# Kernel optimization log

Hardware: AMD Instinct MI355X
Metric: run time of the kernel (lower is better)

Reference implementation:

```python
import jax, jax.numpy as jnp
import numpy as np

NUM_GRAPHS = 64
NODE_SZ = 200
FEAT = 200
HID = 256          # hidden_size; each signed branch outputs HID//2
HALF = HID // 2
N_NODES = NUM_GRAPHS * NODE_SZ
N_EDGES = 409600
NUM_LAYERS = 3


def _lin_init(key, out_f, in_f):
    kw, kb = jax.random.split(key)
    s = 1.0 / np.sqrt(in_f)
    W = jax.random.uniform(kw, (out_f, in_f), minval=-s, maxval=s, dtype=jnp.float32)
    b = jax.random.uniform(kb, (out_f,), minval=-s, maxval=s, dtype=jnp.float32)
    return W, b


def setup_inputs() -> dict:
    key = jax.random.key(0)
    ks = jax.random.split(key, 16)
    x = jax.random.normal(ks[0], (N_NODES, FEAT), dtype=jnp.float32)
    edge_index = jax.random.randint(ks[1], (2, N_EDGES), 0, N_NODES, dtype=jnp.int64)
    edge_weight = jax.random.normal(ks[2], (N_EDGES,), dtype=jnp.float32)
    batch = jnp.repeat(jnp.arange(NUM_GRAPHS, dtype=jnp.int64), NODE_SZ)

    # signed conv layer params: layer0 in=FEAT, layers 1..: in=HID; each lin maps 2*in -> HALF
    Wp0, bp0 = _lin_init(ks[3], HALF, 2 * FEAT)
    Wn0, bn0 = _lin_init(ks[4], HALF, 2 * FEAT)
    Wp1, bp1 = _lin_init(ks[5], HALF, 2 * HID)
    Wn1, bn1 = _lin_init(ks[6], HALF, 2 * HID)
    Wp2, bp2 = _lin_init(ks[7], HALF, 2 * HID)
    Wn2, bn2 = _lin_init(ks[8], HALF, 2 * HID)
    Wr, br = _lin_init(ks[9], HID, NODE_SZ * HID)   # readout_lin
    Wl, bl = _lin_init(ks[10], 1, HID)              # final lin
    return dict(x=x, edge_index=edge_index, edge_weight=edge_weight, batch=batch,
                Wp0=Wp0, bp0=bp0, Wn0=Wn0, bn0=bn0,
                Wp1=Wp1, bp1=bp1, Wn1=Wn1, bn1=bn1,
                Wp2=Wp2, bp2=bp2, Wn2=Wn2, bn2=bn2,
                Wr=Wr, br=br, Wl=Wl, bl=bl)


def _signed_conv(x, src, dst, w, Wp, bp, Wn, bn):
    # edge-weighted signed mean aggregation, split by weight sign
    xs = x[src]                                   # [E, D] gather
    pw = jnp.where(w > 0, w, 0.0)
    nw = jnp.where(w < 0, -w, 0.0)
    agg_p = jax.ops.segment_sum(pw[:, None] * xs, dst, num_segments=N_NODES)
    agg_n = jax.ops.segment_sum(nw[:, None] * xs, dst, num_segments=N_NODES)
    deg_p = jax.ops.segment_sum((w > 0).astype(x.dtype), dst, num_segments=N_NODES)
    deg_n = jax.ops.segment_sum((w < 0).astype(x.dtype), dst, num_segments=N_NODES)
    agg_p = agg_p / jnp.maximum(deg_p, 1.0)[:, None]
    agg_n = agg_n / jnp.maximum(deg_n, 1.0)[:, None]
    hp = jnp.concatenate([agg_p, x], -1) @ Wp.T + bp
    hn = jnp.concatenate([agg_n, x], -1) @ Wn.T + bn
    return jnp.concatenate([hp, hn], -1)          # [N, HID]


def reference(x, edge_index, edge_weight, batch,
              Wp0, bp0, Wn0, bn0, Wp1, bp1, Wn1, bn1, Wp2, bp2, Wn2, bn2,
              Wr, br, Wl, bl):
    src, dst = edge_index[0], edge_index[1]
    convs = [(Wp0, bp0, Wn0, bn0), (Wp1, bp1, Wn1, bn1), (Wp2, bp2, Wn2, bn2)]
    h = x
    for i, (Wp, bp, Wn, bn) in enumerate(convs):
        h = _signed_conv(h, src, dst, edge_weight, Wp, bp, Wn, bn)
        if i < NUM_LAYERS - 1:
            h = jax.nn.leaky_relu(h, negative_slope=0.01)
    # per-graph readout: batch is contiguous with NODE_SZ nodes per graph,
    # so the boolean-mask+view loop is exactly a reshape.
    g = h.reshape(NUM_GRAPHS, NODE_SZ * HID)
    g = g @ Wr.T + br                             # [G, HID]
    # dropout(p=0.5) is identity in eval mode
    return g @ Wl.T + bl                          # [G, 1]
```

## Files before the change

### kernel.cpp

```cpp
#include <hip/hip_runtime.h>

#define NUM_GRAPHS 64
#define NODE_SZ    200
#define FEAT       200
#define HID        256
#define HALF       128
#define N_NODES    (NUM_GRAPHS * NODE_SZ)
#define KREAD      (NODE_SZ * HID)

typedef unsigned short ushort_t;
typedef unsigned int uint_t;
typedef __attribute__((ext_vector_type(8))) short bf16x8;
typedef __attribute__((ext_vector_type(4))) float f32x4;

#define GAS(p) ((const __attribute__((address_space(1))) void*)(p))
#define LAS(p) ((__attribute__((address_space(3))) void*)(p))

__device__ __forceinline__ float bf2f(ushort_t u) {
    union { unsigned int i; float f; } v; v.i = ((unsigned int)u) << 16; return v.f;
}
__device__ __forceinline__ ushort_t f2bf(float f) {
    union { float f; unsigned int i; } v; v.f = f;
    unsigned int x = v.i;
    unsigned int r = (x + 0x7fffu + ((x >> 16) & 1u)) >> 16;
    return (ushort_t)r;
}

#define OFF_CNT    0
#define OFF_WEFF   51264
#define OFF_ES     256064
#define OFF_YALL   13363264
#define OFF_HA     26470464
#define OFF_HB     33024064
#define OFF_WALL   39577664
#define OFF_XB     40364096

__global__ __launch_bounds__(256) void prep_kernel(
        const float* __restrict__ Wp0, const float* __restrict__ Wn0,
        const float* __restrict__ Wp1, const float* __restrict__ Wn1,
        const float* __restrict__ Wp2, const float* __restrict__ Wn2,
        const float* __restrict__ x, const float* __restrict__ Wr,
        const float* __restrict__ Wl, const float* __restrict__ br,
        const float* __restrict__ bl,
        ushort_t* __restrict__ wall, ushort_t* __restrict__ xb,
        float* __restrict__ weff, float* __restrict__ outg) {
    int bx = blockIdx.x, tid = threadIdx.x;
    if (bx < 200) {
        int k = bx * 256 + tid;
        float s[16];
#pragma unroll
        for (int j = 0; j < 16; ++j) s[j] = 0.f;
#pragma unroll 1
        for (int c = 0; c < 256; c += 16) {
#pragma unroll
            for (int j = 0; j < 16; ++j)
                s[j] = fmaf(Wl[c + j], Wr[(size_t)(c + j) * KREAD + k], s[j]);
        }
        float t0 = ((s[0] + s[1]) + (s[2] + s[3])) + ((s[4] + s[5]) + (s[6] + s[7]));
        float t1 = ((s[8] + s[9]) + (s[10] + s[11])) + ((s[12] + s[13]) + (s[14] + s[15]));
        weff[k] = t0 + t1;
    } else if (bx < 300) {
        for (int idx = (bx - 200) * 256 + tid; idx < N_NODES * 64; idx += 25600) {
            int n = idx >> 6, c0 = (idx & 63) * 4;
            ushort4 o = {0, 0, 0, 0};
            if (c0 < 200) {
                float4 v = *(const float4*)&x[(size_t)n * 200 + c0];
                o.x = f2bf(v.x); o.y = f2bf(v.y); o.z = f2bf(v.z); o.w = f2bf(v.w);
            }
            *(ushort4*)&xb[(size_t)n * 256 + c0] = o;
        }
    } else if (bx < 364) {
        for (int idx = (bx - 300) * 256 + tid; idx < 3 * 131072; idx += 16384) {
            int layer = idx >> 17, within = idx & 131071;
            int rr = within >> 8, col = within & 255;
            const float* Wp = (layer == 0) ? Wp0 : (layer == 1) ? Wp1 : Wp2;
            const float* Wn = (layer == 0) ? Wn0 : (layer == 1) ? Wn1 : Wn2;
            int Ks = (layer == 0) ? 200 : 256;
            int q = rr >> 7;
            const float* Wsrc = (q & 1) ? Wn : Wp;
            int row = rr & 127;
            int scol = col + ((q >> 1) ? Ks : 0);
            float v = (col < Ks) ? Wsrc[(size_t)row * (2 * Ks) + scol] : 0.0f;
            wall[idx] = f2bf(v);
        }
    } else {
        if (tid < 64) {
            float p = br[tid] * Wl[tid] + br[tid + 64] * Wl[tid + 64]
                    + br[tid + 128] * Wl[tid + 128] + br[tid + 192] * Wl[tid + 192];
#pragma unroll
            for (int d = 32; d > 0; d >>= 1) p += __shfl_xor(p, d);
            outg[tid] = p + bl[0];
        }
    }
}

__device__ __forceinline__ void gemm_body(int t, const ushort_t* __restrict__ A,
                                          const ushort_t* __restrict__ Bw,
                                          ushort_t* __restrict__ Y,
                                          ushort_t* smem) {
    int mBase = (t >> 1) * 128;
    int nBase = (t & 1) * 256;
    int tid  = threadIdx.x;
    int lane = tid & 63;
    int wv   = tid >> 6;
    int r    = lane & 15;
    int quad = lane >> 4;
    int wm   = wv >> 1;
    int wn   = wv & 1;

    int rowA = tid >> 2, colc = (tid & 3) * 8;
    const ushort_t* gA  = A  + (size_t)(mBase + rowA) * 256 + colc;
    const ushort_t* gB0 = Bw + (size_t)(nBase + rowA) * 256 + colc;
    const ushort_t* gB1 = Bw + (size_t)(nBase + 128 + rowA) * 256 + colc;

    f32x4 acc[2][8];
#pragma unroll
    for (int i = 0; i < 2; ++i)
#pragma unroll
        for (int j = 0; j < 8; ++j) acc[i][j] = (f32x4){0.f, 0.f, 0.f, 0.f};

    auto STAGE = [&](int buf, int kb) {
        ushort_t* Ad = smem + (buf << 12) + tid * 8;
        ushort_t* Bd = smem + 8192 + (buf << 13) + tid * 8;
        __builtin_amdgcn_global_load_lds(GAS(gA + kb), LAS(Ad), 16, 0, 0);
        __builtin_amdgcn_global_load_lds(GAS(gB0 + kb), LAS(Bd), 16, 0, 0);
        __builtin_amdgcn_global_load_lds(GAS(gB1 + kb), LAS(Bd + 4096), 16, 0, 0);
    };

    STAGE(0, 0);
    for (int kt = 0; kt < 8; ++kt) {
        int cb = kt & 1;
        __syncthreads();
        if (kt < 7) STAGE(cb ^ 1, (kt + 1) * 32);
        const ushort_t* Ac = smem + (cb << 12);
        const ushort_t* Bc = smem + 8192 + (cb << 13);
        bf16x8 af[2];
#pragma unroll
        for (int i = 0; i < 2; ++i)
            af[i] = *(const bf16x8*)&Ac[(wm * 32 + i * 16 + r) * 32 + quad * 8];
#pragma unroll
        for (int j = 0; j < 8; ++j) {
            bf16x8 bfr = *(const bf16x8*)&Bc[(wn * 128 + j * 16 + r) * 32 + quad * 8];
            acc[0][j] = __builtin_amdgcn_mfma_f32_16x16x32_bf16(af[0], bfr, acc[0][j], 0, 0, 0);
            acc[1][j] = __builtin_amdgcn_mfma_f32_16x16x32_bf16(af[1], bfr, acc[1][j], 0, 0, 0);
        }
    }
#pragma unroll
    for (int i = 0; i < 2; ++i)
#pragma unroll
        for (int j = 0; j < 8; ++j) {
            int c = nBase + wn * 128 + j * 16 + r;
#pragma unroll
            for (int reg = 0; reg < 4; ++reg) {
                int m = mBase + wm * 32 + i * 16 + quad * 4 + reg;
                Y[(size_t)m * 512 + c] = f2bf(acc[i][j][reg]);
            }
        }
}

__global__ __launch_bounds__(512) void scatgemm_kernel(
        const int* __restrict__ ei, const float* __restrict__ ew,
        uint_t* __restrict__ cnt, uint2* __restrict__ es, int E,
        const ushort_t* __restrict__ xb, const ushort_t* __restrict__ wall,
        ushort_t* __restrict__ Yall) {
    __shared__ __align__(16) ushort_t smem[24576];
    int bx = blockIdx.x;
    if (bx < 200) {
        gemm_body(bx, xb, wall, Yall, smem);
        return;
    }
    int e = (bx - 200) * 512 + threadIdx.x;
    if (e < E) {
        int src = ei[e];
        int dst = ei[E + e];
        float w = ew[e];
        if (w > 0.0f) {
            uint_t old = atomicAdd(&cnt[dst], 1u);
            uint_t rk = old & 0xffffu;
            if (rk < 64u)
                es[(size_t)dst * 128 + rk] = make_uint2((uint_t)src, __float_as_uint(w));
        } else if (w < 0.0f) {
            uint_t old = atomicAdd(&cnt[dst], 0x10000u);
            uint_t rk = old >> 16;
            if (rk < 64u)
                es[(size_t)dst * 128 + 64 + rk] = make_uint2((uint_t)src, __float_as_uint(-w));
        }
    }
}

__global__ __launch_bounds__(512) void gemm_kernel(const ushort_t* __restrict__ A,
                                                   const ushort_t* __restrict__ Bw,
                                                   ushort_t* __restrict__ Y) {
    __shared__ __align__(16) ushort_t smem[24576];
    gemm_body(blockIdx.x, A, Bw, Y, smem);
}

template <int B, bool CLAMP>
__device__ __forceinline__ void gather_batch(const uint2* __restrict__ esb,
                                             uint_t e, uint_t hi,
                                             const ushort_t* __restrict__ Yph, int c0,
                                             float* __restrict__ acc) {
    uint_t u[B];
    float  w[B];
#pragma unroll
    for (int j = 0; j < B; ++j) {
        uint_t idx = CLAMP ? min(e + (uint_t)j, hi - 1u) : (e + (uint_t)j);
        uint2 r = esb[idx];
        uint_t s = __builtin_amdgcn_readfirstlane(r.x);
        float  wj = __uint_as_float(r.y);
        w[j] = (CLAMP && (e + (uint_t)j >= hi)) ? 0.0f : wj;
        u[j] = *(const uint_t*)&Yph[(size_t)s * 512 + c0];
    }
#pragma unroll
    for (int j = 0; j < B; ++j) {
        acc[0] = fmaf(w[j], bf2f((ushort_t)(u[j] & 0xffffu)), acc[0]);
        acc[1] = fmaf(w[j], bf2f((ushort_t)(u[j] >> 16)), acc[1]);
    }
}

template <bool LEAKY, bool DOT>
__global__ __launch_bounds__(256) void agg_kernel(
        const ushort_t* __restrict__ Y,
        const uint_t* __restrict__ cnt,
        const uint2* __restrict__ es,
        const float* __restrict__ bp, const float* __restrict__ bn,
        ushort_t* __restrict__ outp,
        const float* __restrict__ weff,
        float* __restrict__ outg) {
    __shared__ float sdot[4];
    int lane = threadIdx.x & 63;
    int wv   = threadIdx.x >> 6;
    int n = blockIdx.x * 4 + wv;
    int c0 = lane * 2;
    uint_t c = __builtin_amdgcn_readfirstlane(cnt[n]);
    uint_t kp = c & 0xffffu, kn = c >> 16;

    float accp[2] = {0.f, 0.f};
    float accn[2] = {0.f, 0.f};

#pragma unroll 1
    for (int phase = 0; phase < 2; ++phase) {
        uint_t hi = phase ? kn : kp;
        const uint2* esb = es + (size_t)n * 128 + (phase ? 64 : 0);
        float* acc = phase ? accn : accp;
        const ushort_t* Yph = Y + (phase ? 128 : 0);
        uint_t e = 0;
#pragma unroll 1
        while (e + 16 <= hi) { gather_batch<16, false>(esb, e, hi, Yph, c0, acc); e += 16; }
        if (e + 8 <= hi)     { gather_batch<8,  false>(esb, e, hi, Yph, c0, acc); e += 8; }
        if (e < hi)          { gather_batch<8,  true >(esb, e, hi, Yph, c0, acc); }
    }

    float dp = fmaxf((float)kp, 1.0f);
    float dn = fmaxf((float)kn, 1.0f);
    float rp = 1.0f / dp, rn = 1.0f / dn;
    uint_t zp = *(const uint_t*)&Y[(size_t)n * 512 + 256 + c0];
    uint_t zn = *(const uint_t*)&Y[(size_t)n * 512 + 384 + c0];
    float vp0 = fmaf(accp[0], rp, bf2f((ushort_t)(zp & 0xffffu)) + bp[c0]);
    float vp1 = fmaf(accp[1], rp, bf2f((ushort_t)(zp >> 16))     + bp[c0 + 1]);
    float vn0 = fmaf(accn[0], rn, bf2f((ushort_t)(zn & 0xffffu)) + bn[c0]);
    float vn1 = fmaf(accn[1], rn, bf2f((ushort_t)(zn >> 16))     + bn[c0 + 1]);
    if (LEAKY) {
        vp0 = (vp0 > 0.0f) ? vp0 : 0.01f * vp0;
        vp1 = (vp1 > 0.0f) ? vp1 : 0.01f * vp1;
        vn0 = (vn0 > 0.0f) ? vn0 : 0.01f * vn0;
        vn1 = (vn1 > 0.0f) ? vn1 : 0.01f * vn1;
    }
    if (DOT) {
        int g = blockIdx.x / 50;
        int kbase = (n % 200) * 256;
        float s = vp0 * weff[kbase + c0] + vp1 * weff[kbase + c0 + 1]
                + vn0 * weff[kbase + 128 + c0] + vn1 * weff[kbase + 128 + c0 + 1];
#pragma unroll
        for (int d = 32; d > 0; d >>= 1) s += __shfl_xor(s, d);
        if (lane == 0) sdot[wv] = s;
        __syncthreads();
        if (threadIdx.x == 0)
            atomicAdd(&outg[g], (sdot[0] + sdot[1]) + (sdot[2] + sdot[3]));
    } else {
        uint_t op = (uint_t)f2bf(vp0) | ((uint_t)f2bf(vp1) << 16);
        uint_t on = (uint_t)f2bf(vn0) | ((uint_t)f2bf(vn1) << 16);
        *(uint_t*)&outp[(size_t)n * 256 + c0]       = op;
        *(uint_t*)&outp[(size_t)n * 256 + 128 + c0] = on;
    }
}

extern "C" void kernel_launch(void* const* d_in, const int* in_sizes, int n_in,
                              void* d_out, int out_size, void* d_ws, size_t ws_size,
                              hipStream_t stream) {
    const float* x  = (const float*)d_in[0];
    const int*   ei = (const int*)d_in[1];
    const float* ew = (const float*)d_in[2];
    const float* Wp0 = (const float*)d_in[4];
    const float* bp0 = (const float*)d_in[5];
    const float* Wn0 = (const float*)d_in[6];
    const float* bn0 = (const float*)d_in[7];
    const float* Wp1 = (const float*)d_in[8];
    const float* bp1 = (const float*)d_in[9];
    const float* Wn1 = (const float*)d_in[10];
    const float* bn1 = (const float*)d_in[11];
    const float* Wp2 = (const float*)d_in[12];
    const float* bp2 = (const float*)d_in[13];
    const float* Wn2 = (const float*)d_in[14];
    const float* bn2 = (const float*)d_in[15];
    const float* Wr  = (const float*)d_in[16];
    const float* br  = (const float*)d_in[17];
    const float* Wl  = (const float*)d_in[18];
    const float* bl  = (const float*)d_in[19];
    const int E = in_sizes[1] / 2;

    char* ws = (char*)d_ws;
    uint_t*   cnt    = (uint_t*)(ws + OFF_CNT);
    float*    weff   = (float*)(ws + OFF_WEFF);
    uint2*    es     = (uint2*)(ws + OFF_ES);
    ushort_t* Yall   = (ushort_t*)(ws + OFF_YALL);
    ushort_t* hA     = (ushort_t*)(ws + OFF_HA);
    ushort_t* hB     = (ushort_t*)(ws + OFF_HB);
    ushort_t* wall   = (ushort_t*)(ws + OFF_WALL);
    ushort_t* xb     = (ushort_t*)(ws + OFF_XB);
    float*    outg   = (float*)d_out;

    hipMemsetAsync(ws + OFF_CNT, 0, N_NODES * sizeof(uint_t), stream);
    hipLaunchKernelGGL(prep_kernel, dim3(365), dim3(256), 0, stream,
                       Wp0, Wn0, Wp1, Wn1, Wp2, Wn2, x, Wr, Wl, br, bl,
                       wall, xb, weff, outg);
    hipLaunchKernelGGL(scatgemm_kernel, dim3(200 + (E + 511) / 512), dim3(512), 0, stream,
                       ei, ew, cnt, es, E, xb, wall, Yall);
    hipLaunchKernelGGL((agg_kernel<true, false>), dim3(N_NODES / 4), dim3(256), 0, stream,
                       Yall, cnt, es, bp0, bn0, hA, (const float*)nullptr, (float*)nullptr);
    hipLaunchKernelGGL(gemm_kernel, dim3(200), dim3(512), 0, stream, hA, wall + 131072, Yall);
    hipLaunchKernelGGL((agg_kernel<true, false>), dim3(N_NODES / 4), dim3(256), 0, stream,
                       Yall, cnt, es, bp1, bn1, hB, (const float*)nullptr, (float*)nullptr);
    hipLaunchKernelGGL(gemm_kernel, dim3(200), dim3(512), 0, stream, hB, wall + 262144, Yall);
    hipLaunchKernelGGL((agg_kernel<false, true>), dim3(N_NODES / 4), dim3(256), 0, stream,
                       Yall, cnt, es, bp2, bn2, (ushort_t*)nullptr, weff, outg);
}
```

Baseline: 285.2 us.

## Process positive and negative edge lists concurrently in half-wavefronts with 8-byte gathers

Splits each 64-lane wavefront in the aggregation kernel into two halves: one gathers positive-weight neighbours and the other negative-weight neighbours at the same time, each lane covering 4 bf16 columns through an 8-byte load. This replaces running the two phases one after the other with 2 columns per lane. The aim is to halve the serial gather loop length and widen each memory access. In exchange the edge source index is no longer wave-uniform (the readfirstlane is dropped), and the loop runs to max(kp,kn), so the half with fewer edges wastes iterations on clamped, zero-weighted loads.

```diff
diff --git a/kernel.cpp b/kernel.cpp
--- a/kernel.cpp
+++ b/kernel.cpp
@@ -195,29 +195,6 @@
     gemm_body(blockIdx.x, A, Bw, Y, smem);
 }
 
-template <int B, bool CLAMP>
-__device__ __forceinline__ void gather_batch(const uint2* __restrict__ esb,
-                                             uint_t e, uint_t hi,
-                                             const ushort_t* __restrict__ Yph, int c0,
-                                             float* __restrict__ acc) {
-    uint_t u[B];
-    float  w[B];
-#pragma unroll
-    for (int j = 0; j < B; ++j) {
-        uint_t idx = CLAMP ? min(e + (uint_t)j, hi - 1u) : (e + (uint_t)j);
-        uint2 r = esb[idx];
-        uint_t s = __builtin_amdgcn_readfirstlane(r.x);
-        float  wj = __uint_as_float(r.y);
-        w[j] = (CLAMP && (e + (uint_t)j >= hi)) ? 0.0f : wj;
-        u[j] = *(const uint_t*)&Yph[(size_t)s * 512 + c0];
-    }
-#pragma unroll
-    for (int j = 0; j < B; ++j) {
-        acc[0] = fmaf(w[j], bf2f((ushort_t)(u[j] & 0xffffu)), acc[0]);
-        acc[1] = fmaf(w[j], bf2f((ushort_t)(u[j] >> 16)), acc[1]);
-    }
-}
-
 template <bool LEAKY, bool DOT>
 __global__ __launch_bounds__(256) void agg_kernel(
         const ushort_t* __restrict__ Y,
@@ -231,57 +208,74 @@
     int lane = threadIdx.x & 63;
     int wv   = threadIdx.x >> 6;
     int n = blockIdx.x * 4 + wv;
-    int c0 = lane * 2;
+    int half = lane >> 5;
+    int hl   = lane & 31;
+    int c0   = hl * 4;
     uint_t c = __builtin_amdgcn_readfirstlane(cnt[n]);
     uint_t kp = c & 0xffffu, kn = c >> 16;
-
-    float accp[2] = {0.f, 0.f};
-    float accn[2] = {0.f, 0.f};
+    uint_t kh = half ? kn : kp;
+    uint_t himax = max(kp, kn);
+
+    const uint2* esb = es + (size_t)n * 128 + (half ? 64 : 0);
+    const ushort_t* Yph = Y + half * 128 + c0;
+
+    float acc[4] = {0.f, 0.f, 0.f, 0.f};
+    uint_t clampi = (kh > 0u) ? (kh - 1u) : 0u;
 
 #pragma unroll 1
-    for (int phase = 0; phase < 2; ++phase) {
-        uint_t hi = phase ? kn : kp;
-        const uint2* esb = es + (size_t)n * 128 + (phase ? 64 : 0);
-        float* acc = phase ? accn : accp;
-        const ushort_t* Yph = Y + (phase ? 128 : 0);
-        uint_t e = 0;
-#pragma unroll 1
-        while (e + 16 <= hi) { gather_batch<16, false>(esb, e, hi, Yph, c0, acc); e += 16; }
-        if (e + 8 <= hi)     { gather_batch<8,  false>(esb, e, hi, Yph, c0, acc); e += 8; }
-        if (e < hi)          { gather_batch<8,  true >(esb, e, hi, Yph, c0, acc); }
-    }
-
-    float dp = fmaxf((float)kp, 1.0f);
-    float dn = fmaxf((float)kn, 1.0f);
-    float rp = 1.0f / dp, rn = 1.0f / dn;
-    uint_t zp = *(const uint_t*)&Y[(size_t)n * 512 + 256 + c0];
-    uint_t zn = *(const uint_t*)&Y[(size_t)n * 512 + 384 + c0];
-    float vp0 = fmaf(accp[0], rp, bf2f((ushort_t)(zp & 0xffffu)) + bp[c0]);
-    float vp1 = fmaf(accp[1], rp, bf2f((ushort_t)(zp >> 16))     + bp[c0 + 1]);
-    float vn0 = fmaf(accn[0], rn, bf2f((ushort_t)(zn & 0xffffu)) + bn[c0]);
-    float vn1 = fmaf(accn[1], rn, bf2f((ushort_t)(zn >> 16))     + bn[c0 + 1]);
+    for (uint_t e = 0; e < himax; e += 8) {
+        uint2 u[8];
+        float w[8];
+#pragma unroll
+        for (int j = 0; j < 8; ++j) {
+            uint_t idx = e + (uint_t)j;
+            uint2 r = esb[min(idx, clampi)];
+            w[j] = (idx < kh) ? __uint_as_float(r.y) : 0.0f;
+            uint_t s = min(r.x, (uint_t)(N_NODES - 1));
+            u[j] = *(const uint2*)&Yph[(size_t)s * 512];
+        }
+#pragma unroll
+        for (int j = 0; j < 8; ++j) {
+            const ushort_t* q = (const ushort_t*)&u[j];
+            acc[0] = fmaf(w[j], bf2f(q[0]), acc[0]);
+            acc[1] = fmaf(w[j], bf2f(q[1]), acc[1]);
+            acc[2] = fmaf(w[j], bf2f(q[2]), acc[2]);
+            acc[3] = fmaf(w[j], bf2f(q[3]), acc[3]);
+        }
+    }
+
+    float d = fmaxf((float)kh, 1.0f);
+    float rcp = 1.0f / d;
+    uint2 z = *(const uint2*)&Y[(size_t)n * 512 + 256 + half * 128 + c0];
+    const ushort_t* zq = (const ushort_t*)&z;
+    const float* bb = half ? bn : bp;
+    float4 bv = *(const float4*)&bb[c0];
+    float v0 = fmaf(acc[0], rcp, bf2f(zq[0]) + bv.x);
+    float v1 = fmaf(acc[1], rcp, bf2f(zq[1]) + bv.y);
+    float v2 = fmaf(acc[2], rcp, bf2f(zq[2]) + bv.z);
+    float v3 = fmaf(acc[3], rcp, bf2f(zq[3]) + bv.w);
     if (LEAKY) {
-        vp0 = (vp0 > 0.0f) ? vp0 : 0.01f * vp0;
-        vp1 = (vp1 > 0.0f) ? vp1 : 0.01f * vp1;
-        vn0 = (vn0 > 0.0f) ? vn0 : 0.01f * vn0;
-        vn1 = (vn1 > 0.0f) ? vn1 : 0.01f * vn1;
+        v0 = (v0 > 0.0f) ? v0 : 0.01f * v0;
+        v1 = (v1 > 0.0f) ? v1 : 0.01f * v1;
+        v2 = (v2 > 0.0f) ? v2 : 0.01f * v2;
+        v3 = (v3 > 0.0f) ? v3 : 0.01f * v3;
     }
     if (DOT) {
         int g = blockIdx.x / 50;
-        int kbase = (n % 200) * 256;
-        float s = vp0 * weff[kbase + c0] + vp1 * weff[kbase + c0 + 1]
-                + vn0 * weff[kbase + 128 + c0] + vn1 * weff[kbase + 128 + c0 + 1];
-#pragma unroll
-        for (int d = 32; d > 0; d >>= 1) s += __shfl_xor(s, d);
+        int kbase = (n % 200) * 256 + half * 128 + c0;
+        float4 wf = *(const float4*)&weff[kbase];
+        float s = v0 * wf.x + v1 * wf.y + v2 * wf.z + v3 * wf.w;
+#pragma unroll
+        for (int dd = 32; dd > 0; dd >>= 1) s += __shfl_xor(s, dd);
         if (lane == 0) sdot[wv] = s;
         __syncthreads();
         if (threadIdx.x == 0)
             atomicAdd(&outg[g], (sdot[0] + sdot[1]) + (sdot[2] + sdot[3]));
     } else {
-        uint_t op = (uint_t)f2bf(vp0) | ((uint_t)f2bf(vp1) << 16);
-        uint_t on = (uint_t)f2bf(vn0) | ((uint_t)f2bf(vn1) << 16);
-        *(uint_t*)&outp[(size_t)n * 256 + c0]       = op;
-        *(uint_t*)&outp[(size_t)n * 256 + 128 + c0] = on;
+        uint2 o;
+        o.x = (uint_t)f2bf(v0) | ((uint_t)f2bf(v1) << 16);
+        o.y = (uint_t)f2bf(v2) | ((uint_t)f2bf(v3) << 16);
+        *(uint2*)&outp[(size_t)n * 256 + half * 128 + c0] = o;
     }
 }
 
```

Result: slower. 293.3 us (+2.8%).
